# Kernel tuning notes

Hardware: AMD Instinct MI355X
Metric: run time of the kernel (lower is better)

The kernel has to match this reference:

```python
import jax, jax.numpy as jnp
import numpy as np

TWO_PI = np.float32(2.0 * np.pi)


def setup_inputs() -> dict:
    H, W = 2048, 2048
    MAX_COC = 21  # gain_params['max_CoC']
    key = jax.random.key(0)
    k1, k2 = jax.random.split(key)
    image = jax.random.uniform(k1, (H, W, 3), dtype=jnp.float32)
    # per-pixel circle-of-confusion kernel size (what GetSparseTensor derives from the depth map)
    kernel_size_flatten = jax.random.randint(k2, (H * W,), 0, MAX_COC + 1, dtype=jnp.int32)
    return {"image": image, "kernel_size_flatten": kernel_size_flatten, "max_coc": MAX_COC}


def reference(image, kernel_size_flatten, max_coc):
    """Spatially-variant Gaussian defocus blur.

    Faithful to CudaGetDefocusWeightsKernel: each input pixel px with
    kernel_size k > 1 scatters image[px] * N(offset; sigma=k/6) to all
    in-bounds neighbors within k//2; pixels with k <= 1 pass through
    (weight 1.0 at themselves). Out-of-bounds targets are skipped (the
    kernel clamps the loop range), realized here by a discarded padding
    ring on the output buffer.
    """
    H, W, C = image.shape
    half_max = max_coc // 2  # static Python int

    ks = kernel_size_flatten.reshape(H, W)            # [H, W] int
    half_k = (ks // 2).astype(jnp.float32)            # kernel_size // 2
    blur = ks > 1                                     # [H, W] bool
    sigma = ks.astype(jnp.float32) / 6.0
    sigma_safe = jnp.where(blur, sigma, 1.0)          # avoid 0-div on identity pixels
    inv_2s2 = 0.5 / (sigma_safe * sigma_safe)         # [H, W]
    norm = 1.0 / (TWO_PI * sigma_safe * sigma_safe)   # [H, W]

    offs = jnp.arange(-half_max, half_max + 1)
    dys, dxs = jnp.meshgrid(offs, offs, indexing="ij")
    dys, dxs = dys.reshape(-1), dxs.reshape(-1)       # [K^2] scatter offsets

    pad = half_max
    out0 = jnp.zeros((H + 2 * pad, W + 2 * pad, C), image.dtype)

    def step(out, off):
        dy, dx = off
        d2 = (dy * dy + dx * dx).astype(jnp.float32)
        in_win = (jnp.abs(dy).astype(jnp.float32) <= half_k) & (
            jnp.abs(dx).astype(jnp.float32) <= half_k
        )
        gw = jnp.exp(-d2 * inv_2s2) * norm            # [H, W] Gaussian weight
        wmap = jnp.where(blur & in_win, gw, 0.0)
        wmap = jnp.where((~blur) & (dy == 0) & (dx == 0), 1.0, wmap)
        contrib = image * wmap[..., None]             # [H, W, C]
        y0, x0 = pad + dy, pad + dx
        cur = jax.lax.dynamic_slice(out, (y0, x0, 0), (H, W, C))
        out = jax.lax.dynamic_update_slice(out, cur + contrib, (y0, x0, 0))
        return out, None

    out, _ = jax.lax.scan(step, out0, (dys, dxs))
    return out[pad:pad + H, pad:pad + W, :]
```

## Files before the change

kernel.cpp:

```cpp
#include <hip/hip_runtime.h>
#include <hip/hip_fp16.h>

#define IMG_W 2048
#define IMG_H 2048
#define HALF  10
#define TILE_H 32
#define TILE_W 64
#define LH (TILE_H + 2*HALF)
#define LW (TILE_W + 2*HALF)
#define NSTG (LH * LW)

#define L_KSD 37
#define L_NDW (22 * L_KSD)

__device__ __forceinline__ __half2 h2(uint u)  { union { uint a; __half2 b; } c; c.a = u; return c.b; }
__device__ __forceinline__ uint pack2(float a, float b) {
    return (uint)__half_as_ushort(__float2half(a)) |
           ((uint)__half_as_ushort(__float2half(b)) << 16);
}
__device__ __forceinline__ int swz(int c) {
    return c ^ (((c >> 2) + (c >> 4)) & 3);
}

__device__ __forceinline__ float wyv(int k, int oy) {
    int a = abs(oy), hk = k >> 1;
    if (a > hk) return 0.f;
    if (k <= 1) return 1.f;
    float kk = (float)(k * k);
    return expf(-(float)(oy * oy) * 18.f / kk) * 5.7295780f / kk;
}
__device__ __forceinline__ float wxv(int k, int ox) {
    int a = abs(ox), hk = k >> 1;
    if (a > hk) return 0.f;
    if (k <= 1) return 1.f;
    float kk = (float)(k * k);
    return expf(-(float)(ox * ox) * 18.f / kk);
}

__global__ __launch_bounds__(256)
void defocus_sep_kernel(const float* __restrict__ img,
                        const int* __restrict__ ks,
                        float* __restrict__ out)
{
    __shared__ uint  lutw[L_NDW];
    __shared__ uint2 tile[NSTG];

    const int tid = threadIdx.x;
    const int X0 = blockIdx.x * TILE_W;
    const int Y0 = blockIdx.y * TILE_H;

    for (int i = tid; i < L_NDW; i += 256) {
        int k = i / L_KSD;
        int d = i - k * L_KSD;
        float lo, hi;
        if (d < 22) {
            lo = wyv(k, d - 10);
            hi = wyv(k, d - 11);
        } else {
            int pos = (d - 22) * 2;
            lo = wxv(k, pos - 13);
            hi = wxv(k, pos - 12);
        }
        lutw[i] = pack2(lo, hi);
    }

    for (int i = tid; i < NSTG; i += 256) {
        int r = i / LW;
        int c = i - r * LW;
        int gy = Y0 - HALF + r;
        int gx = X0 - HALF + c;
        float fr = 0.f, fg = 0.f, fb = 0.f;
        uint kp = 0;
        if (gy >= 0 && gy < IMG_H && gx >= 0 && gx < IMG_W) {
            int p = gy * IMG_W + gx;
            fr = img[p * 3 + 0];
            fg = img[p * 3 + 1];
            fb = img[p * 3 + 2];
            kp = (uint)(ks[p] * L_KSD);
        }
        uint2 v;
        v.x = pack2(fr, fg);
        v.y = (pack2(fb, 0.f) & 0xffffu) | (kp << 16);
        tile[r * LW + swz(c)] = v;
    }
    __syncthreads();

    const int tx = tid & 15;
    const int ty = tid >> 4;
    const int colbase = tx * 4;
    const int rowbase = ty * 2;

    int pxidx[24];
    #pragma unroll
    for (int b = 0; b < 24; ++b) pxidx[b] = swz(colbase + b);

    const __half2 hz = h2(0u);
    __half2 a32[2][3], a10[2][3];
    float mc[2][4][3];
    #pragma unroll
    for (int r = 0; r < 2; ++r)
        #pragma unroll
        for (int c = 0; c < 3; ++c) {
            a32[r][c] = hz; a10[r][c] = hz;
            mc[r][0][c] = mc[r][1][c] = mc[r][2][c] = mc[r][3][c] = 0.f;
        }

#define ROW(aa)                                                                    \
    { const int rowoff = (rowbase + (aa)) * LW;                                    \
      _Pragma("unroll")                                                            \
      for (int b = 0; b < 24; ++b) {                                               \
          uint2 p = tile[rowoff + pxidx[b]];                                       \
          __half2 hx = h2(p.x), hy = h2(p.y);                                      \
          __half2 rr = __low2half2(hx), gg = __high2half2(hx), bb = __low2half2(hy); \
          const int wb = (int)(p.y >> 16);                                         \
          __half2 wy2 = h2(lutw[wb + (aa)]);                                       \
          __half2 wy0 = __low2half2(wy2), wy1 = __high2half2(wy2);                 \
          const int h = b >> 1;                                                    \
          uint w32, w10;    \
          if ((b & 1) == 0) {                                                      \
              w32 = lutw[wb + 22 + h];                                             \
              w10 = lutw[wb + 23 + h];                                             \
          } else {                                                                 \
              uint q0 = lutw[wb + 22 + h];                                         \
              uint q1 = lutw[wb + 23 + h];                                         \
              uint q2 = lutw[wb + 24 + h];                                         \
              w32 = __builtin_amdgcn_alignbit(q1, q0, 16);                         \
              w10 = __builtin_amdgcn_alignbit(q2, q1, 16);                         \
          }                                                                        \
          __half2 W320 = __hmul2(h2(w32), wy0), W100 = __hmul2(h2(w10), wy0);      \
          __half2 W321 = __hmul2(h2(w32), wy1), W101 = __hmul2(h2(w10), wy1);      \
          a32[0][0] = __hfma2(rr, W320, a32[0][0]);                                \
          a32[0][1] = __hfma2(gg, W320, a32[0][1]);                                \
          a32[0][2] = __hfma2(bb, W320, a32[0][2]);                                \
          a10[0][0] = __hfma2(rr, W100, a10[0][0]);                                \
          a10[0][1] = __hfma2(gg, W100, a10[0][1]);                                \
          a10[0][2] = __hfma2(bb, W100, a10[0][2]);                                \
          a32[1][0] = __hfma2(rr, W321, a32[1][0]);                                \
          a32[1][1] = __hfma2(gg, W321, a32[1][1]);                                \
          a32[1][2] = __hfma2(bb, W321, a32[1][2]);                                \
          a10[1][0] = __hfma2(rr, W101, a10[1][0]);                                \
          a10[1][1] = __hfma2(gg, W101, a10[1][1]);                                \
          a10[1][2] = __hfma2(bb, W101, a10[1][2]);                                \
      } }

#define FLUSH()                                                        \
    { _Pragma("unroll")                                                \
      for (int r = 0; r < 2; ++r) {                                    \
          _Pragma("unroll")                                            \
          for (int c = 0; c < 3; ++c) {                                \
              float2 f3 = __half22float2(a32[r][c]);                   \
              float2 f1 = __half22float2(a10[r][c]);                   \
              mc[r][3][c] += f3.x; mc[r][2][c] += f3.y;                \
              mc[r][1][c] += f1.x; mc[r][0][c] += f1.y;                \
              a32[r][c] = hz; a10[r][c] = hz;                          \
          }                                                            \
      } }

    #pragma unroll 1
    for (int ap = 0; ap < 11; ++ap) {
        ROW(2 * ap);
        ROW(2 * ap + 1);
        FLUSH();
    }

    #pragma unroll
    for (int r = 0; r < 2; ++r) {
        int gy = Y0 + rowbase + r;
        #pragma unroll
        for (int m = 0; m < 4; ++m) {
            int gx = X0 + colbase + m;
            int o = (gy * IMG_W + gx) * 3;
            out[o + 0] = mc[r][m][0];
            out[o + 1] = mc[r][m][1];
            out[o + 2] = mc[r][m][2];
        }
    }
#undef ROW
#undef FLUSH
}

extern "C" void kernel_launch(void* const* d_in, const int* in_sizes, int n_in,
                              void* d_out, int out_size, void* d_ws, size_t ws_size,
                              hipStream_t stream) {
    const float* img = (const float*)d_in[0];
    const int*   ks  = (const int*)d_in[1];
    float* out = (float*)d_out;

    dim3 grid(IMG_W / TILE_W, IMG_H / TILE_H);
    dim3 block(256);
    defocus_sep_kernel<<<grid, block, 0, stream>>>(img, ks, out);
}
```

Baseline: 200.6 us.

## Precompute odd-shifted weight LUT and use byte-offset immediate LDS addressing

Extends the per-k weight LUT with a second, half-shifted copy of the horizontal weights, so odd pixel positions read pre-aligned pairs instead of doing three loads plus alignbit. The tile stores a byte offset into the LUT and uses a strided column layout (c&3)*21+(c>>2) in place of the XOR swizzle, which removes the per-thread index array and lets loads use constant immediate offsets. This lowers LDS instruction count and register use at the cost of a larger LUT and possible new bank-conflict patterns.

```diff
diff --git a/kernel.cpp b/kernel.cpp
--- a/kernel.cpp
+++ b/kernel.cpp
@@ -10,7 +10,8 @@
 #define LW (TILE_W + 2*HALF)
 #define NSTG (LH * LW)
 
-#define L_KSD 37
+#define L_KSD 51
+#define L_KSB 204
 #define L_NDW (22 * L_KSD)
 
 __device__ __forceinline__ __half2 h2(uint u)  { union { uint a; __half2 b; } c; c.a = u; return c.b; }
@@ -18,10 +19,6 @@
     return (uint)__half_as_ushort(__float2half(a)) |
            ((uint)__half_as_ushort(__float2half(b)) << 16);
 }
-__device__ __forceinline__ int swz(int c) {
-    return c ^ (((c >> 2) + (c >> 4)) & 3);
-}
-
 __device__ __forceinline__ float wyv(int k, int oy) {
     int a = abs(oy), hk = k >> 1;
     if (a > hk) return 0.f;
@@ -38,11 +35,11 @@
 }
 
 __global__ __launch_bounds__(256)
-void defocus_sep_kernel(const float* __restrict__ img,
+void defocus_imm_kernel(const float* __restrict__ img,
                         const int* __restrict__ ks,
                         float* __restrict__ out)
 {
-    __shared__ uint  lutw[L_NDW];
+    __shared__ uint  lutw[L_NDW + 2];
     __shared__ uint2 tile[NSTG];
 
     const int tid = threadIdx.x;
@@ -52,14 +49,18 @@
     for (int i = tid; i < L_NDW; i += 256) {
         int k = i / L_KSD;
         int d = i - k * L_KSD;
-        float lo, hi;
+        float lo = 0.f, hi = 0.f;
         if (d < 22) {
             lo = wyv(k, d - 10);
             hi = wyv(k, d - 11);
-        } else {
-            int pos = (d - 22) * 2;
-            lo = wxv(k, pos - 13);
-            hi = wxv(k, pos - 12);
+        } else if (d < 36) {
+            int j = d - 22;
+            lo = wxv(k, 2 * j - 13);
+            hi = wxv(k, 2 * j - 12);
+        } else if (d < 50) {
+            int j = d - 36;
+            lo = wxv(k, 2 * j - 12);
+            hi = wxv(k, 2 * j - 11);
         }
         lutw[i] = pack2(lo, hi);
     }
@@ -70,18 +71,18 @@
         int gy = Y0 - HALF + r;
         int gx = X0 - HALF + c;
         float fr = 0.f, fg = 0.f, fb = 0.f;
-        uint kp = 0;
+        uint koffB = 0;
         if (gy >= 0 && gy < IMG_H && gx >= 0 && gx < IMG_W) {
             int p = gy * IMG_W + gx;
             fr = img[p * 3 + 0];
             fg = img[p * 3 + 1];
             fb = img[p * 3 + 2];
-            kp = (uint)(ks[p] * L_KSD);
+            koffB = (uint)(ks[p] * L_KSB);
         }
         uint2 v;
         v.x = pack2(fr, fg);
-        v.y = (pack2(fb, 0.f) & 0xffffu) | (kp << 16);
-        tile[r * LW + swz(c)] = v;
+        v.y = koffB | ((uint)__half_as_ushort(__float2half(fb)) << 16);
+        tile[r * LW + (c & 3) * 21 + (c >> 2)] = v;
     }
     __syncthreads();
 
@@ -89,10 +90,7 @@
     const int ty = tid >> 4;
     const int colbase = tx * 4;
     const int rowbase = ty * 2;
-
-    int pxidx[24];
-    #pragma unroll
-    for (int b = 0; b < 24; ++b) pxidx[b] = swz(colbase + b);
+    const int pxbase  = rowbase * LW + tx;
 
     const __half2 hz = h2(0u);
     __half2 a32[2][3], a10[2][3];
@@ -106,26 +104,21 @@
         }
 
 #define ROW(aa)                                                                    \
-    { const int rowoff = (rowbase + (aa)) * LW;                                    \
-      _Pragma("unroll")                                                            \
+    { _Pragma("unroll")                                                            \
       for (int b = 0; b < 24; ++b) {                                               \
-          uint2 p = tile[rowoff + pxidx[b]];                                       \
+          uint2 p = tile[pxbase + (aa) * LW + (b & 3) * 21 + (b >> 2)];            \
           __half2 hx = h2(p.x), hy = h2(p.y);                                      \
-          __half2 rr = __low2half2(hx), gg = __high2half2(hx), bb = __low2half2(hy); \
-          const int wb = (int)(p.y >> 16);                                         \
-          __half2 wy2 = h2(lutw[wb + (aa)]);                                       \
+          __half2 rr = __low2half2(hx), gg = __high2half2(hx), bb = __high2half2(hy); \
+          const char* wp = (const char*)lutw + (p.y & 0xffffu);                    \
+          __half2 wy2 = h2(*(const uint*)(wp + 4 * (aa)));                         \
           __half2 wy0 = __low2half2(wy2), wy1 = __high2half2(wy2);                 \
-          const int h = b >> 1;                                                    \
           uint w32, w10;    \
           if ((b & 1) == 0) {                                                      \
-              w32 = lutw[wb + 22 + h];                                             \
-              w10 = lutw[wb + 23 + h];                                             \
+              w32 = *(const uint*)(wp + 4 * (22 + (b >> 1)));                      \
+              w10 = *(const uint*)(wp + 4 * (23 + (b >> 1)));                      \
           } else {                                                                 \
-              uint q0 = lutw[wb + 22 + h];                                         \
-              uint q1 = lutw[wb + 23 + h];                                         \
-              uint q2 = lutw[wb + 24 + h];                                         \
-              w32 = __builtin_amdgcn_alignbit(q1, q0, 16);                         \
-              w10 = __builtin_amdgcn_alignbit(q2, q1, 16);                         \
+              w32 = *(const uint*)(wp + 4 * (36 + ((b - 1) >> 1)));                \
+              w10 = *(const uint*)(wp + 4 * (36 + ((b + 1) >> 1)));                \
           }                                                                        \
           __half2 W320 = __hmul2(h2(w32), wy0), W100 = __hmul2(h2(w10), wy0);      \
           __half2 W321 = __hmul2(h2(w32), wy1), W101 = __hmul2(h2(w10), wy1);      \
@@ -188,5 +181,5 @@
 
     dim3 grid(IMG_W / TILE_W, IMG_H / TILE_H);
     dim3 block(256);
-    defocus_sep_kernel<<<grid, block, 0, stream>>>(img, ks, out);
+    defocus_imm_kernel<<<grid, block, 0, stream>>>(img, ks, out);
 }
```

Measured after the change: 194.1 us. 3.2% less time.
